# Performance work log

Measured on AMD Instinct MI355X. Metric: run time of the kernel, lower is better.

## Reference

```python
import jax, jax.numpy as jnp
import numpy as np

N = 500_000
H_DIM = 256
G_DIM = 256
NUM_GRAPHS = 8192


def setup_inputs() -> dict:
    key = jax.random.key(0)
    k_h, k_b, k_w = jax.random.split(key, 3)
    h = jax.random.normal(k_h, (N, H_DIM), dtype=jnp.float32)
    batch = jnp.sort(jax.random.randint(k_b, (N,), 0, NUM_GRAPHS, dtype=jnp.int64))
    # Linear(h_dim*4, g_dim): weight [g_dim, 4*h_dim] in torch; we store as [4*h_dim, g_dim]
    fan_in = 4 * H_DIM
    bound = 1.0 / np.sqrt(fan_in)
    W = jax.random.uniform(k_w, (4 * H_DIM, G_DIM), minval=-bound, maxval=bound, dtype=jnp.float32)
    b = jnp.zeros((G_DIM,), dtype=jnp.float32)
    return {"h": h, "batch": batch, "W": W, "b": b, "num_graphs": NUM_GRAPHS}


def reference(h, batch, W, b, num_graphs):
    G = num_graphs
    ones = jnp.ones((h.shape[0],), dtype=h.dtype)
    cnt = jax.ops.segment_sum(ones, batch, num_segments=G)            # [G]
    s = jax.ops.segment_sum(h, batch, num_segments=G)                 # [G, D]
    ssq = jax.ops.segment_sum(h * h, batch, num_segments=G)           # [G, D]
    safe_cnt = jnp.maximum(cnt, 1.0)[:, None]
    h_mean = s / safe_cnt                                             # scatter mean (0 for empty)
    nonempty = (cnt > 0)[:, None]
    h_min = jnp.where(nonempty, jax.ops.segment_min(h, batch, num_segments=G), 0.0)
    h_max = jnp.where(nonempty, jax.ops.segment_max(h, batch, num_segments=G), 0.0)
    # unbiased std as in torch_scatter.scatter_std: var = (sum_sq - mean*sum) / (count - 1)
    var = (ssq - h_mean * s) / jnp.maximum(cnt - 1.0, 1.0)[:, None]
    h_std = jnp.sqrt(jnp.maximum(var, 0.0))
    hc = jnp.concatenate([h_mean, h_min, h_max, h_std], axis=1)       # [G, 4D]
    return hc @ W + b                                                 # [G, g_dim]
```

## Files before the change

kernel.cpp:

```cpp
#include <hip/hip_runtime.h>
#include <hip/hip_bf16.h>


#define DIM 256
#define NG 8192
#define KD 1024
#define NOUT 256

typedef __attribute__((ext_vector_type(8))) short bf16x8;
typedef __attribute__((ext_vector_type(4))) float f32x4;

__device__ __forceinline__ unsigned short f2bf(float x) {
    unsigned int u = __float_as_uint(x);
    u += 0x7fffu + ((u >> 16) & 1u);
    return (unsigned short)(u >> 16);
}

__device__ __forceinline__ unsigned int pack2(float a, float b) {
    return (unsigned int)f2bf(a) | ((unsigned int)f2bf(b) << 16);
}

__global__ __launch_bounds__(256) void prep_kernel(const float* __restrict__ W,
                                                   const int* __restrict__ batch,
                                                   int N,
                                                   unsigned short* __restrict__ WT,
                                                   int* __restrict__ offs) {
    __shared__ float tile[64][68];

    if (blockIdx.x >= 64) {
        int t = ((int)blockIdx.x - 64) * 256 + (int)threadIdx.x;
        if (t > NG) return;
        const bool is64 = (batch[N - 1] == 0);
        int lo = 0, hi = N;
        while (lo < hi) {
            int mid = (lo + hi) >> 1;
            int v = is64 ? batch[2 * mid] : batch[mid];
            if (v < t) lo = mid + 1; else hi = mid;
        }
        offs[t] = lo;
        return;
    }

    const int t = threadIdx.x;
    const int tk0 = ((int)blockIdx.x & 15) * 64;
    const int tn0 = ((int)blockIdx.x >> 4) * 64;
    const int lk = t >> 2;
    const int ln = (t & 3) * 16;
#pragma unroll
    for (int j = 0; j < 16; j += 4) {
        float4 v = *(const float4*)&W[(size_t)(tk0 + lk) * NOUT + tn0 + ln + j];
        *(float4*)&tile[lk][ln + j] = v;
    }
    __syncthreads();
    const int on = t >> 2;
    const int ok = (t & 3) * 16;
    unsigned short tmp[16];
#pragma unroll
    for (int j = 0; j < 16; ++j) tmp[j] = f2bf(tile[ok + j][on]);
    const int n = tn0 + on;
    const int ct = n >> 4;
    const int c = n & 15;
    const int o0 = (tk0 + ok) >> 3;
    bf16x8 lo8, hi8;
#pragma unroll
    for (int j = 0; j < 8; ++j) { lo8[j] = (short)tmp[j]; hi8[j] = (short)tmp[8 + j]; }
    *(bf16x8*)&WT[(size_t)(((ct * 128 + o0) * 16 + c)) * 8]     = lo8;
    *(bf16x8*)&WT[(size_t)(((ct * 128 + o0 + 1) * 16 + c)) * 8] = hi8;
}

__global__ __launch_bounds__(256, 4) void fused_kernel(const float* __restrict__ h,
                                                       const int* __restrict__ offs,
                                                       const unsigned short* __restrict__ BT,
                                                       const float* __restrict__ bias,
                                                       float* __restrict__ out) {
    __shared__ unsigned short As[16 * 1024];
    const int w = threadIdx.x >> 6;
    const int lane = threadIdx.x & 63;
    const int tile = blockIdx.x;
    const int g0 = tile * 16 + w * 4;

    const int ob = offs[g0 + (lane < 5 ? lane : 4)];
    const f32x4* __restrict__ hv = (const f32x4*)h;

    for (int i = 0; i < 4; ++i) {
        const int start = __shfl(ob, i);
        const int end = __shfl(ob, i + 1);

        float s0[4] = {0.f,0.f,0.f,0.f}, s1[4] = {0.f,0.f,0.f,0.f};
        float q0[4] = {0.f,0.f,0.f,0.f}, q1[4] = {0.f,0.f,0.f,0.f};
        float mn[4] = {INFINITY, INFINITY, INFINITY, INFINITY};
        float mx[4] = {-INFINITY, -INFINITY, -INFINITY, -INFINITY};

        int r = start;
        for (; r + 8 <= end; r += 8) {
            f32x4 v[8];
#pragma unroll
            for (int j = 0; j < 8; ++j)
                v[j] = __builtin_nontemporal_load(hv + (size_t)(r + j) * 64 + lane);
#pragma unroll
            for (int j = 0; j < 8; ++j) {
                if (j & 1) {
#pragma unroll
                    for (int i2 = 0; i2 < 4; ++i2) {
                        s1[i2] += v[j][i2]; q1[i2] = fmaf(v[j][i2], v[j][i2], q1[i2]);
                        mn[i2] = fminf(mn[i2], v[j][i2]); mx[i2] = fmaxf(mx[i2], v[j][i2]);
                    }
                } else {
#pragma unroll
                    for (int i2 = 0; i2 < 4; ++i2) {
                        s0[i2] += v[j][i2]; q0[i2] = fmaf(v[j][i2], v[j][i2], q0[i2]);
                        mn[i2] = fminf(mn[i2], v[j][i2]); mx[i2] = fmaxf(mx[i2], v[j][i2]);
                    }
                }
            }
        }
        for (; r < end; ++r) {
            f32x4 a = __builtin_nontemporal_load(hv + (size_t)r * 64 + lane);
#pragma unroll
            for (int i2 = 0; i2 < 4; ++i2) {
                s0[i2] += a[i2]; q0[i2] = fmaf(a[i2], a[i2], q0[i2]);
                mn[i2] = fminf(mn[i2], a[i2]); mx[i2] = fmaxf(mx[i2], a[i2]);
            }
        }

        const int cnt = end - start;
        const float cf = (float)cnt;
        const float inv = cnt > 0 ? 1.f / cf : 0.f;
        const float invm1 = 1.f / fmaxf(cf - 1.f, 1.f);
        float mean[4], sd[4];
#pragma unroll
        for (int i2 = 0; i2 < 4; ++i2) {
            float s = s0[i2] + s1[i2];
            float q = q0[i2] + q1[i2];
            mean[i2] = s * inv;
            float var = (q - mean[i2] * s) * invm1;
            sd[i2] = sqrtf(fmaxf(var, 0.f));
            if (cnt == 0) { mn[i2] = 0.f; mx[i2] = 0.f; }
        }

        const int lr = w * 4 + i;
        const unsigned int rx = (unsigned int)((lr & 7) << 4);
        char* base = (char*)As;
        const unsigned int b0 = (unsigned int)(lr * 2048 + lane * 8);
        *(uint2*)(base + ((b0 + 0)    ^ rx)) = make_uint2(pack2(mean[0], mean[1]), pack2(mean[2], mean[3]));
        *(uint2*)(base + ((b0 + 512)  ^ rx)) = make_uint2(pack2(mn[0], mn[1]),     pack2(mn[2], mn[3]));
        *(uint2*)(base + ((b0 + 1024) ^ rx)) = make_uint2(pack2(mx[0], mx[1]),     pack2(mx[2], mx[3]));
        *(uint2*)(base + ((b0 + 1536) ^ rx)) = make_uint2(pack2(sd[0], sd[1]),     pack2(sd[2], sd[3]));
    }

    __syncthreads();

    const int fr = lane & 15;
    const int gq = lane >> 4;
    const unsigned int arx = (unsigned int)((fr & 7) << 4);
    const unsigned int abase = (unsigned int)(fr * 2048 + gq * 16);

    f32x4 acc[4] = {{0.f,0.f,0.f,0.f},{0.f,0.f,0.f,0.f},{0.f,0.f,0.f,0.f},{0.f,0.f,0.f,0.f}};

    const unsigned short* Bb[4];
#pragma unroll
    for (int fc = 0; fc < 4; ++fc)
        Bb[fc] = BT + ((((size_t)(w * 4 + fc) * 128 + gq) * 16 + fr) << 3);

#pragma unroll 2
    for (int t = 0; t < 32; ++t) {
        bf16x8 af = *(const bf16x8*)((const char*)As + ((abase + t * 64) ^ arx));
#pragma unroll
        for (int fc = 0; fc < 4; ++fc) {
            bf16x8 bfr = *(const bf16x8*)(Bb[fc] + t * 512);
            acc[fc] = __builtin_amdgcn_mfma_f32_16x16x32_bf16(af, bfr, acc[fc], 0, 0, 0);
        }
    }

    const size_t row0 = (size_t)tile * 16;
#pragma unroll
    for (int fc = 0; fc < 4; ++fc) {
        int col = w * 64 + fc * 16 + fr;
        float bv = bias[col];
#pragma unroll
        for (int e = 0; e < 4; ++e) {
            size_t row = row0 + gq * 4 + e;
            out[row * NOUT + col] = acc[fc][e] + bv;
        }
    }
}

extern "C" void kernel_launch(void* const* d_in, const int* in_sizes, int n_in,
                              void* d_out, int out_size, void* d_ws, size_t ws_size,
                              hipStream_t stream) {
    const float* h     = (const float*)d_in[0];
    const int*   batch = (const int*)d_in[1];
    const float* W     = (const float*)d_in[2];
    const float* b     = (const float*)d_in[3];
    float* out = (float*)d_out;

    const int N = in_sizes[0] / DIM;

    char* ws = (char*)d_ws;
    unsigned short* WT = (unsigned short*)ws;
    int* offs = (int*)(ws + 524288);

    prep_kernel<<<97, 256, 0, stream>>>(W, batch, N, WT, offs);
    fused_kernel<<<NG / 16, 256, 0, stream>>>(h, offs, WT, b, out);
}
```

Measured before the change: 99.35 us.

## Stream each wave's four segments as one contiguous row range with inline flushes

Each wave now walks the whole contiguous row range covering its four graphs in one loop of 8-row unrolled loads, flushing the statistics to shared memory whenever it crosses a segment boundary. The old version ran a separate loop per graph, each with its own scalar tail, which left short loops and poor load batching at every graph edge. The launch-bounds occupancy hint is also dropped. The cost is a data-dependent flush check inside the unrolled loop, which may add branch overhead or raise register pressure and lower occupancy.

```diff
diff --git a/kernel.cpp b/kernel.cpp
--- a/kernel.cpp
+++ b/kernel.cpp
@@ -68,11 +68,11 @@
     *(bf16x8*)&WT[(size_t)(((ct * 128 + o0 + 1) * 16 + c)) * 8] = hi8;
 }
 
-__global__ __launch_bounds__(256, 4) void fused_kernel(const float* __restrict__ h,
-                                                       const int* __restrict__ offs,
-                                                       const unsigned short* __restrict__ BT,
-                                                       const float* __restrict__ bias,
-                                                       float* __restrict__ out) {
+__global__ __launch_bounds__(256) void fused_kernel(const float* __restrict__ h,
+                                                    const int* __restrict__ offs,
+                                                    const unsigned short* __restrict__ BT,
+                                                    const float* __restrict__ bias,
+                                                    float* __restrict__ out) {
     __shared__ unsigned short As[16 * 1024];
     const int w = threadIdx.x >> 6;
     const int lane = threadIdx.x & 63;
@@ -80,73 +80,87 @@
     const int g0 = tile * 16 + w * 4;
 
     const int ob = offs[g0 + (lane < 5 ? lane : 4)];
-    const f32x4* __restrict__ hv = (const f32x4*)h;
-
-    for (int i = 0; i < 4; ++i) {
-        const int start = __shfl(ob, i);
-        const int end = __shfl(ob, i + 1);
-
-        float s0[4] = {0.f,0.f,0.f,0.f}, s1[4] = {0.f,0.f,0.f,0.f};
-        float q0[4] = {0.f,0.f,0.f,0.f}, q1[4] = {0.f,0.f,0.f,0.f};
-        float mn[4] = {INFINITY, INFINITY, INFINITY, INFINITY};
-        float mx[4] = {-INFINITY, -INFINITY, -INFINITY, -INFINITY};
-
-        int r = start;
-        for (; r + 8 <= end; r += 8) {
-            f32x4 v[8];
-#pragma unroll
-            for (int j = 0; j < 8; ++j)
-                v[j] = __builtin_nontemporal_load(hv + (size_t)(r + j) * 64 + lane);
-#pragma unroll
-            for (int j = 0; j < 8; ++j) {
-                if (j & 1) {
-#pragma unroll
-                    for (int i2 = 0; i2 < 4; ++i2) {
-                        s1[i2] += v[j][i2]; q1[i2] = fmaf(v[j][i2], v[j][i2], q1[i2]);
-                        mn[i2] = fminf(mn[i2], v[j][i2]); mx[i2] = fmaxf(mx[i2], v[j][i2]);
-                    }
-                } else {
-#pragma unroll
-                    for (int i2 = 0; i2 < 4; ++i2) {
-                        s0[i2] += v[j][i2]; q0[i2] = fmaf(v[j][i2], v[j][i2], q0[i2]);
-                        mn[i2] = fminf(mn[i2], v[j][i2]); mx[i2] = fmaxf(mx[i2], v[j][i2]);
-                    }
-                }
-            }
-        }
-        for (; r < end; ++r) {
-            f32x4 a = __builtin_nontemporal_load(hv + (size_t)r * 64 + lane);
-#pragma unroll
-            for (int i2 = 0; i2 < 4; ++i2) {
-                s0[i2] += a[i2]; q0[i2] = fmaf(a[i2], a[i2], q0[i2]);
-                mn[i2] = fminf(mn[i2], a[i2]); mx[i2] = fmaxf(mx[i2], a[i2]);
-            }
-        }
-
-        const int cnt = end - start;
+    const int wave_start = __shfl(ob, 0);
+    const int wave_end = __shfl(ob, 4);
+
+    float s0[4] = {0.f,0.f,0.f,0.f}, s1[4] = {0.f,0.f,0.f,0.f};
+    float q0[4] = {0.f,0.f,0.f,0.f}, q1[4] = {0.f,0.f,0.f,0.f};
+    float mn[4] = {INFINITY, INFINITY, INFINITY, INFINITY};
+    float mx[4] = {-INFINITY, -INFINITY, -INFINITY, -INFINITY};
+
+    int bidx = 0;
+    int seg_start = wave_start;
+    int next_b = __shfl(ob, 1);
+
+    char* lbase = (char*)As;
+    auto flush = [&]() {
+        const int bend = __shfl(ob, bidx + 1);
+        const int cnt = bend - seg_start;
         const float cf = (float)cnt;
         const float inv = cnt > 0 ? 1.f / cf : 0.f;
         const float invm1 = 1.f / fmaxf(cf - 1.f, 1.f);
         float mean[4], sd[4];
 #pragma unroll
-        for (int i2 = 0; i2 < 4; ++i2) {
-            float s = s0[i2] + s1[i2];
-            float q = q0[i2] + q1[i2];
-            mean[i2] = s * inv;
-            float var = (q - mean[i2] * s) * invm1;
-            sd[i2] = sqrtf(fmaxf(var, 0.f));
-            if (cnt == 0) { mn[i2] = 0.f; mx[i2] = 0.f; }
-        }
-
-        const int lr = w * 4 + i;
+        for (int i = 0; i < 4; ++i) {
+            float s = s0[i] + s1[i];
+            float q = q0[i] + q1[i];
+            mean[i] = s * inv;
+            float var = (q - mean[i] * s) * invm1;
+            sd[i] = sqrtf(fmaxf(var, 0.f));
+            if (cnt == 0) { mn[i] = 0.f; mx[i] = 0.f; }
+        }
+        const int lr = w * 4 + bidx;
         const unsigned int rx = (unsigned int)((lr & 7) << 4);
-        char* base = (char*)As;
         const unsigned int b0 = (unsigned int)(lr * 2048 + lane * 8);
-        *(uint2*)(base + ((b0 + 0)    ^ rx)) = make_uint2(pack2(mean[0], mean[1]), pack2(mean[2], mean[3]));
-        *(uint2*)(base + ((b0 + 512)  ^ rx)) = make_uint2(pack2(mn[0], mn[1]),     pack2(mn[2], mn[3]));
-        *(uint2*)(base + ((b0 + 1024) ^ rx)) = make_uint2(pack2(mx[0], mx[1]),     pack2(mx[2], mx[3]));
-        *(uint2*)(base + ((b0 + 1536) ^ rx)) = make_uint2(pack2(sd[0], sd[1]),     pack2(sd[2], sd[3]));
-    }
+        *(uint2*)(lbase + ((b0 + 0)    ^ rx)) = make_uint2(pack2(mean[0], mean[1]), pack2(mean[2], mean[3]));
+        *(uint2*)(lbase + ((b0 + 512)  ^ rx)) = make_uint2(pack2(mn[0], mn[1]),     pack2(mn[2], mn[3]));
+        *(uint2*)(lbase + ((b0 + 1024) ^ rx)) = make_uint2(pack2(mx[0], mx[1]),     pack2(mx[2], mx[3]));
+        *(uint2*)(lbase + ((b0 + 1536) ^ rx)) = make_uint2(pack2(sd[0], sd[1]),     pack2(sd[2], sd[3]));
+#pragma unroll
+        for (int i = 0; i < 4; ++i) {
+            s0[i] = 0.f; s1[i] = 0.f; q0[i] = 0.f; q1[i] = 0.f;
+            mn[i] = INFINITY; mx[i] = -INFINITY;
+        }
+        seg_start = bend;
+        ++bidx;
+        next_b = __shfl(ob, bidx < 4 ? bidx + 1 : 4);
+    };
+
+    const f32x4* __restrict__ hv = (const f32x4*)h;
+    int r = wave_start;
+    for (; r + 8 <= wave_end; r += 8) {
+        f32x4 v[8];
+#pragma unroll
+        for (int j = 0; j < 8; ++j)
+            v[j] = __builtin_nontemporal_load(hv + (size_t)(r + j) * 64 + lane);
+#pragma unroll
+        for (int j = 0; j < 8; ++j) {
+            while (r + j == next_b && bidx < 3) flush();
+            if (j & 1) {
+#pragma unroll
+                for (int i = 0; i < 4; ++i) {
+                    s1[i] += v[j][i]; q1[i] = fmaf(v[j][i], v[j][i], q1[i]);
+                    mn[i] = fminf(mn[i], v[j][i]); mx[i] = fmaxf(mx[i], v[j][i]);
+                }
+            } else {
+#pragma unroll
+                for (int i = 0; i < 4; ++i) {
+                    s0[i] += v[j][i]; q0[i] = fmaf(v[j][i], v[j][i], q0[i]);
+                    mn[i] = fminf(mn[i], v[j][i]); mx[i] = fmaxf(mx[i], v[j][i]);
+                }
+            }
+        }
+    }
+    for (; r < wave_end; ++r) {
+        f32x4 a = __builtin_nontemporal_load(hv + (size_t)r * 64 + lane);
+        while (r == next_b && bidx < 3) flush();
+#pragma unroll
+        for (int i = 0; i < 4; ++i) {
+            s0[i] += a[i]; q0[i] = fmaf(a[i], a[i], q0[i]);
+            mn[i] = fminf(mn[i], a[i]); mx[i] = fmaxf(mx[i], a[i]);
+        }
+    }
+    while (bidx < 4) flush();
 
     __syncthreads();
 
```

Result: no change. 97.95 us (-1.4%).

## Double-buffer two graph tiles per block and interleave GEMM with streaming

Applied to the files above, without the earlier changes.

Each block now handles 32 graphs as two 16-graph tiles with double-buffered LDS. MFMA steps for the first tile run inside the row-streaming loop of the second, so matrix work overlaps the memory-bound reduction. Each wave also streams all rows of its four graphs in one contiguous loop and flushes segment statistics at boundaries, rather than restarting per graph. This halves the grid (256 blocks), doubles LDS per block and drops the occupancy hint, which may reduce latency hiding on a bandwidth-bound kernel.

```diff
diff --git a/kernel.cpp b/kernel.cpp
--- a/kernel.cpp
+++ b/kernel.cpp
@@ -68,121 +68,157 @@
     *(bf16x8*)&WT[(size_t)(((ct * 128 + o0 + 1) * 16 + c)) * 8] = hi8;
 }
 
-__global__ __launch_bounds__(256, 4) void fused_kernel(const float* __restrict__ h,
-                                                       const int* __restrict__ offs,
-                                                       const unsigned short* __restrict__ BT,
-                                                       const float* __restrict__ bias,
-                                                       float* __restrict__ out) {
-    __shared__ unsigned short As[16 * 1024];
+#define GEMM_STEP(RBUF)                                                        \
+    {                                                                          \
+        bf16x8 af = *(const bf16x8*)((RBUF) + ((abase + kstep * 64) ^ arx));   \
+        _Pragma("unroll")                                                      \
+        for (int fc = 0; fc < 4; ++fc) {                                       \
+            bf16x8 bfr = *(const bf16x8*)(Bb[fc] + kstep * 512);               \
+            acc[fc] = __builtin_amdgcn_mfma_f32_16x16x32_bf16(af, bfr,         \
+                                                              acc[fc], 0, 0, 0);\
+        }                                                                      \
+        ++kstep;                                                               \
+    }
+
+#define WRITE_OUT(ROW0)                                                        \
+    _Pragma("unroll")                                                          \
+    for (int fc = 0; fc < 4; ++fc) {                                           \
+        int col = w * 64 + fc * 16 + fr;                                       \
+        float bv = bias[col];                                                  \
+        _Pragma("unroll")                                                      \
+        for (int e = 0; e < 4; ++e)                                            \
+            out[(size_t)((ROW0) + gq * 4 + e) * NOUT + col] = acc[fc][e] + bv; \
+    }
+
+#define STREAM_TILE(G0, WBUF, INJECT)                                          \
+    {                                                                          \
+        const int ob = offs[(G0) + (lane < 5 ? lane : 4)];                     \
+        const int wave_start = __shfl(ob, 0);                                  \
+        const int wave_end = __shfl(ob, 4);                                    \
+        float s0[4] = {0.f,0.f,0.f,0.f}, s1[4] = {0.f,0.f,0.f,0.f};            \
+        float q0[4] = {0.f,0.f,0.f,0.f}, q1[4] = {0.f,0.f,0.f,0.f};            \
+        float mn[4] = {INFINITY, INFINITY, INFINITY, INFINITY};                 \
+        float mx[4] = {-INFINITY, -INFINITY, -INFINITY, -INFINITY};             \
+        int bidx = 0;                                                          \
+        int seg_start = wave_start;                                            \
+        int next_b = __shfl(ob, 1);                                            \
+        char* lbase = (char*)(WBUF);                                           \
+        auto flush = [&]() {                                                   \
+            const int bend = __shfl(ob, bidx + 1);                             \
+            const int cnt = bend - seg_start;                                  \
+            const float cf = (float)cnt;                                       \
+            const float inv = cnt > 0 ? 1.f / cf : 0.f;                        \
+            const float invm1 = 1.f / fmaxf(cf - 1.f, 1.f);                    \
+            float mean[4], sd[4];                                              \
+            _Pragma("unroll")                                                  \
+            for (int i = 0; i < 4; ++i) {                                      \
+                float s = s0[i] + s1[i];                                       \
+                float q = q0[i] + q1[i];                                       \
+                mean[i] = s * inv;                                             \
+                float var = (q - mean[i] * s) * invm1;                         \
+                sd[i] = sqrtf(fmaxf(var, 0.f));                                \
+                if (cnt == 0) { mn[i] = 0.f; mx[i] = 0.f; }                    \
+            }                                                                  \
+            const int lr = w * 4 + bidx;                                       \
+            const unsigned int rx = (unsigned int)((lr & 7) << 4);             \
+            const unsigned int b0 = (unsigned int)(lr * 2048 + lane * 8);      \
+            *(uint2*)(lbase + ((b0 + 0)    ^ rx)) =                            \
+                make_uint2(pack2(mean[0], mean[1]), pack2(mean[2], mean[3]));  \
+            *(uint2*)(lbase + ((b0 + 512)  ^ rx)) =                            \
+                make_uint2(pack2(mn[0], mn[1]), pack2(mn[2], mn[3]));          \
+            *(uint2*)(lbase + ((b0 + 1024) ^ rx)) =                            \
+                make_uint2(pack2(mx[0], mx[1]), pack2(mx[2], mx[3]));          \
+            *(uint2*)(lbase + ((b0 + 1536) ^ rx)) =                            \
+                make_uint2(pack2(sd[0], sd[1]), pack2(sd[2], sd[3]));          \
+            _Pragma("unroll")                                                  \
+            for (int i = 0; i < 4; ++i) {                                      \
+                s0[i] = 0.f; s1[i] = 0.f; q0[i] = 0.f; q1[i] = 0.f;            \
+                mn[i] = INFINITY; mx[i] = -INFINITY;                           \
+            }                                                                  \
+            seg_start = bend;                                                  \
+            ++bidx;                                                            \
+            next_b = __shfl(ob, bidx < 4 ? bidx + 1 : 4);                      \
+        };                                                                     \
+        int r = wave_start;                                                    \
+        for (; r + 8 <= wave_end; r += 8) {                                    \
+            f32x4 v[8];                                                        \
+            _Pragma("unroll")                                                  \
+            for (int j = 0; j < 8; ++j)                                        \
+                v[j] = __builtin_nontemporal_load(hv + (size_t)(r + j) * 64 + lane); \
+            INJECT;                                                            \
+            _Pragma("unroll")                                                  \
+            for (int j = 0; j < 8; ++j) {                                      \
+                while (r + j == next_b && bidx < 3) flush();                   \
+                if (j & 1) {                                                   \
+                    _Pragma("unroll")                                          \
+                    for (int i = 0; i < 4; ++i) {                              \
+                        s1[i] += v[j][i]; q1[i] = fmaf(v[j][i], v[j][i], q1[i]); \
+                        mn[i] = fminf(mn[i], v[j][i]);                         \
+                        mx[i] = fmaxf(mx[i], v[j][i]);                         \
+                    }                                                          \
+                } else {                                                       \
+                    _Pragma("unroll")                                          \
+                    for (int i = 0; i < 4; ++i) {                              \
+                        s0[i] += v[j][i]; q0[i] = fmaf(v[j][i], v[j][i], q0[i]); \
+                        mn[i] = fminf(mn[i], v[j][i]);                         \
+                        mx[i] = fmaxf(mx[i], v[j][i]);                         \
+                    }                                                          \
+                }                                                              \
+            }                                                                  \
+        }                                                                      \
+        for (; r < wave_end; ++r) {                                            \
+            f32x4 a = __builtin_nontemporal_load(hv + (size_t)r * 64 + lane);  \
+            while (r == next_b && bidx < 3) flush();                           \
+            _Pragma("unroll")                                                  \
+            for (int i = 0; i < 4; ++i) {                                      \
+                s0[i] += a[i]; q0[i] = fmaf(a[i], a[i], q0[i]);                \
+                mn[i] = fminf(mn[i], a[i]); mx[i] = fmaxf(mx[i], a[i]);        \
+            }                                                                  \
+        }                                                                      \
+        while (bidx < 4) flush();                                              \
+    }
+
+__global__ __launch_bounds__(256) void fused_kernel(const float* __restrict__ h,
+                                                    const int* __restrict__ offs,
+                                                    const unsigned short* __restrict__ BT,
+                                                    const float* __restrict__ bias,
+                                                    float* __restrict__ out) {
+    __shared__ unsigned short As[2][16 * 1024];
     const int w = threadIdx.x >> 6;
     const int lane = threadIdx.x & 63;
-    const int tile = blockIdx.x;
-    const int g0 = tile * 16 + w * 4;
-
-    const int ob = offs[g0 + (lane < 5 ? lane : 4)];
+    const int g0 = (int)blockIdx.x * 32 + w * 4;
     const f32x4* __restrict__ hv = (const f32x4*)h;
-
-    for (int i = 0; i < 4; ++i) {
-        const int start = __shfl(ob, i);
-        const int end = __shfl(ob, i + 1);
-
-        float s0[4] = {0.f,0.f,0.f,0.f}, s1[4] = {0.f,0.f,0.f,0.f};
-        float q0[4] = {0.f,0.f,0.f,0.f}, q1[4] = {0.f,0.f,0.f,0.f};
-        float mn[4] = {INFINITY, INFINITY, INFINITY, INFINITY};
-        float mx[4] = {-INFINITY, -INFINITY, -INFINITY, -INFINITY};
-
-        int r = start;
-        for (; r + 8 <= end; r += 8) {
-            f32x4 v[8];
-#pragma unroll
-            for (int j = 0; j < 8; ++j)
-                v[j] = __builtin_nontemporal_load(hv + (size_t)(r + j) * 64 + lane);
-#pragma unroll
-            for (int j = 0; j < 8; ++j) {
-                if (j & 1) {
-#pragma unroll
-                    for (int i2 = 0; i2 < 4; ++i2) {
-                        s1[i2] += v[j][i2]; q1[i2] = fmaf(v[j][i2], v[j][i2], q1[i2]);
-                        mn[i2] = fminf(mn[i2], v[j][i2]); mx[i2] = fmaxf(mx[i2], v[j][i2]);
-                    }
-                } else {
-#pragma unroll
-                    for (int i2 = 0; i2 < 4; ++i2) {
-                        s0[i2] += v[j][i2]; q0[i2] = fmaf(v[j][i2], v[j][i2], q0[i2]);
-                        mn[i2] = fminf(mn[i2], v[j][i2]); mx[i2] = fmaxf(mx[i2], v[j][i2]);
-                    }
-                }
-            }
-        }
-        for (; r < end; ++r) {
-            f32x4 a = __builtin_nontemporal_load(hv + (size_t)r * 64 + lane);
-#pragma unroll
-            for (int i2 = 0; i2 < 4; ++i2) {
-                s0[i2] += a[i2]; q0[i2] = fmaf(a[i2], a[i2], q0[i2]);
-                mn[i2] = fminf(mn[i2], a[i2]); mx[i2] = fmaxf(mx[i2], a[i2]);
-            }
-        }
-
-        const int cnt = end - start;
-        const float cf = (float)cnt;
-        const float inv = cnt > 0 ? 1.f / cf : 0.f;
-        const float invm1 = 1.f / fmaxf(cf - 1.f, 1.f);
-        float mean[4], sd[4];
-#pragma unroll
-        for (int i2 = 0; i2 < 4; ++i2) {
-            float s = s0[i2] + s1[i2];
-            float q = q0[i2] + q1[i2];
-            mean[i2] = s * inv;
-            float var = (q - mean[i2] * s) * invm1;
-            sd[i2] = sqrtf(fmaxf(var, 0.f));
-            if (cnt == 0) { mn[i2] = 0.f; mx[i2] = 0.f; }
-        }
-
-        const int lr = w * 4 + i;
-        const unsigned int rx = (unsigned int)((lr & 7) << 4);
-        char* base = (char*)As;
-        const unsigned int b0 = (unsigned int)(lr * 2048 + lane * 8);
-        *(uint2*)(base + ((b0 + 0)    ^ rx)) = make_uint2(pack2(mean[0], mean[1]), pack2(mean[2], mean[3]));
-        *(uint2*)(base + ((b0 + 512)  ^ rx)) = make_uint2(pack2(mn[0], mn[1]),     pack2(mn[2], mn[3]));
-        *(uint2*)(base + ((b0 + 1024) ^ rx)) = make_uint2(pack2(mx[0], mx[1]),     pack2(mx[2], mx[3]));
-        *(uint2*)(base + ((b0 + 1536) ^ rx)) = make_uint2(pack2(sd[0], sd[1]),     pack2(sd[2], sd[3]));
-    }
-
-    __syncthreads();
 
     const int fr = lane & 15;
     const int gq = lane >> 4;
     const unsigned int arx = (unsigned int)((fr & 7) << 4);
     const unsigned int abase = (unsigned int)(fr * 2048 + gq * 16);
-
-    f32x4 acc[4] = {{0.f,0.f,0.f,0.f},{0.f,0.f,0.f,0.f},{0.f,0.f,0.f,0.f},{0.f,0.f,0.f,0.f}};
-
     const unsigned short* Bb[4];
 #pragma unroll
     for (int fc = 0; fc < 4; ++fc)
         Bb[fc] = BT + ((((size_t)(w * 4 + fc) * 128 + gq) * 16 + fr) << 3);
 
-#pragma unroll 2
-    for (int t = 0; t < 32; ++t) {
-        bf16x8 af = *(const bf16x8*)((const char*)As + ((abase + t * 64) ^ arx));
-#pragma unroll
-        for (int fc = 0; fc < 4; ++fc) {
-            bf16x8 bfr = *(const bf16x8*)(Bb[fc] + t * 512);
-            acc[fc] = __builtin_amdgcn_mfma_f32_16x16x32_bf16(af, bfr, acc[fc], 0, 0, 0);
-        }
-    }
-
-    const size_t row0 = (size_t)tile * 16;
-#pragma unroll
-    for (int fc = 0; fc < 4; ++fc) {
-        int col = w * 64 + fc * 16 + fr;
-        float bv = bias[col];
-#pragma unroll
-        for (int e = 0; e < 4; ++e) {
-            size_t row = row0 + gq * 4 + e;
-            out[row * NOUT + col] = acc[fc][e] + bv;
-        }
-    }
+    f32x4 acc[4];
+    int kstep;
+
+    STREAM_TILE(g0, As[0], {});
+    __syncthreads();
+
+#pragma unroll
+    for (int fc = 0; fc < 4; ++fc) acc[fc] = (f32x4){0.f, 0.f, 0.f, 0.f};
+    kstep = 0;
+    const char* rbuf0 = (const char*)As[0];
+    STREAM_TILE(g0 + 16, As[1], { if (kstep < 32) GEMM_STEP(rbuf0); });
+    while (kstep < 32) GEMM_STEP(rbuf0);
+    WRITE_OUT((size_t)blockIdx.x * 32);
+    __syncthreads();
+
+#pragma unroll
+    for (int fc = 0; fc < 4; ++fc) acc[fc] = (f32x4){0.f, 0.f, 0.f, 0.f};
+    kstep = 0;
+    const char* rbuf1 = (const char*)As[1];
+    while (kstep < 32) GEMM_STEP(rbuf1);
+    WRITE_OUT((size_t)blockIdx.x * 32 + 16);
 }
 
 extern "C" void kernel_launch(void* const* d_in, const int* in_sizes, int n_in,
@@ -201,5 +237,5 @@
     int* offs = (int*)(ws + 524288);
 
     prep_kernel<<<97, 256, 0, stream>>>(W, batch, N, WT, offs);
-    fused_kernel<<<NG / 16, 256, 0, stream>>>(h, offs, WT, b, out);
-}
+    fused_kernel<<<NG / 32, 256, 0, stream>>>(h, offs, WT, b, out);
+}
```

After: 115.2 us. 1.16x slower.
